# Kernel optimization log

Hardware: AMD Instinct MI355X
Metric: run time of the kernel (lower is better)

The kernel has to match this reference:

```python
import jax, jax.numpy as jnp
import numpy as np


def setup_inputs() -> dict:
    key = jax.random.key(0)
    k1, k2 = jax.random.split(key)
    B, P, D = 32, 1024, 384
    x = jax.random.normal(k1, (B, P, D), dtype=jnp.float32)
    durations = jax.random.randint(k2, (B, P), 0, 8, dtype=jnp.int32)
    return {"x": x, "durations": durations, "max_length": 3072}


def reference(x, durations, max_length):
    # x: [B, P, D], durations: [B, P] int
    B, P, D = x.shape
    csum = jnp.cumsum(durations, axis=1)                       # [B, P] inclusive cumsum
    total = csum[:, -1]
    output_lengths = jnp.minimum(total, max_length).astype(jnp.int32)  # clamp like torch.clamp
    T = max_length  # static: durations are chosen so max(output_lengths) == max_length
    t = jnp.arange(T, dtype=jnp.int32)                         # [T] mel frame positions
    # phoneme index for frame t: smallest j with csum[j] > t (skips zero-duration phonemes)
    idx = jax.vmap(lambda c: jnp.searchsorted(c, t, side='right'))(csum)  # [B, T]
    idx = jnp.clip(idx, 0, P - 1)
    out = jnp.take_along_axis(x, idx[:, :, None], axis=1)      # [B, T, D] gather
    mask = t[None, :] < output_lengths[:, None]                # frames past length stay zero
    out = jnp.where(mask[:, :, None], out, jnp.zeros((), dtype=x.dtype))
    return out, output_lengths
```

## Files before the change

kernel.cpp:

```cpp
#include <hip/hip_runtime.h>


#define BB 32
#define PP 1024
#define DD 384
#define TT 3072

__global__ __launch_bounds__(256) void lr_scan_idx_kernel(
    const int* __restrict__ dur, int* __restrict__ idx_map,
    float* __restrict__ len_out)
{
    __shared__ int csum[PP];
    __shared__ int wtot[4];
    const int b    = blockIdx.x;
    const int tid  = threadIdx.x;
    const int lane = tid & 63;
    const int wave = tid >> 6;

    int4 d = ((const int4*)(dur + b * PP))[tid];
    int s0 = d.x;
    int s1 = s0 + d.y;
    int s2 = s1 + d.z;
    int s3 = s2 + d.w;

    int wsum = s3;
    #pragma unroll
    for (int off = 1; off < 64; off <<= 1) {
        int v = __shfl_up(wsum, off, 64);
        if (lane >= off) wsum += v;
    }
    if (lane == 63) wtot[wave] = wsum;
    __syncthreads();

    int woff = 0;
    for (int w = 0; w < wave; ++w) woff += wtot[w];
    const int pre = woff + wsum - s3;

    csum[tid * 4 + 0] = pre + s0;
    csum[tid * 4 + 1] = pre + s1;
    csum[tid * 4 + 2] = pre + s2;
    csum[tid * 4 + 3] = pre + s3;
    __syncthreads();

    const int total  = csum[PP - 1];
    const int outlen = total < TT ? total : TT;
    if (tid == 0) len_out[b] = (float)outlen;

    for (int t = tid; t < TT; t += 256) {
        int m = -1;
        if (t < outlen) {
            int lo = 0, hi = PP;
            while (lo < hi) {
                int mid = (lo + hi) >> 1;
                if (csum[mid] <= t) lo = mid + 1; else hi = mid;
            }
            m = lo;
        }
        idx_map[b * TT + t] = m;
    }
}

__global__ __launch_bounds__(384) void lr_gather_kernel(
    const float* __restrict__ x, const int* __restrict__ idx_map,
    float* __restrict__ out)
{
    const int j   = threadIdx.x;
    const int lr  = j / 96;
    const int c   = j - lr * 96;
    const int b   = blockIdx.y;
    const int t   = blockIdx.x * 4 + lr;
    const int row = b * TT + t;

    const int m = idx_map[row];
    float4 v = make_float4(0.f, 0.f, 0.f, 0.f);
    if (m >= 0) {
        v = ((const float4*)(x + ((size_t)b * PP + m) * DD))[c];
    }
    ((float4*)out)[(size_t)row * 96 + c] = v;
}

extern "C" void kernel_launch(void* const* d_in, const int* in_sizes, int n_in,
                              void* d_out, int out_size, void* d_ws, size_t ws_size,
                              hipStream_t stream) {
    const float* x   = (const float*)d_in[0];
    const int*   dur = (const int*)d_in[1];

    float* out     = (float*)d_out;
    float* len_out = out + (size_t)BB * TT * DD;
    int*   idx_map = (int*)d_ws;

    lr_scan_idx_kernel<<<BB, 256, 0, stream>>>(dur, idx_map, len_out);
    lr_gather_kernel<<<dim3(TT / 4, BB), 384, 0, stream>>>(x, idx_map, out);
}
```

Before: 204.7 us.

## Fuse duration scan and gather into one chunked kernel with scatter-built index

```diff
diff --git a/kernel.cpp b/kernel.cpp
--- a/kernel.cpp
+++ b/kernel.cpp
@@ -5,78 +5,70 @@
 #define PP 1024
 #define DD 384
 #define TT 3072
+#define NCHUNK 16
+#define CHUNK (TT / NCHUNK)
+#define BLOCK 512
+#define NWAVE (BLOCK / 64)
+#define ROW4 (DD / 4)
 
-__global__ __launch_bounds__(256) void lr_scan_idx_kernel(
-    const int* __restrict__ dur, int* __restrict__ idx_map,
-    float* __restrict__ len_out)
+__global__ __launch_bounds__(BLOCK) void lr_fused_kernel(
+    const float* __restrict__ x, const int* __restrict__ dur,
+    float* __restrict__ out, float* __restrict__ len_out)
 {
-    __shared__ int csum[PP];
-    __shared__ int wtot[4];
-    const int b    = blockIdx.x;
+    __shared__ int lidx[CHUNK];
+    __shared__ int wtot[NWAVE];
+
     const int tid  = threadIdx.x;
     const int lane = tid & 63;
-    const int wave = tid >> 6;
+    const int wv   = tid >> 6;
+    const int b    = blockIdx.y;
+    const int lo   = blockIdx.x * CHUNK;
 
-    int4 d = ((const int4*)(dur + b * PP))[tid];
-    int s0 = d.x;
-    int s1 = s0 + d.y;
-    int s2 = s1 + d.z;
-    int s3 = s2 + d.w;
-
-    int wsum = s3;
+    int2 d = ((const int2*)(dur + b * PP))[tid];
+    const int s = d.x + d.y;
+    int wsum = s;
     #pragma unroll
     for (int off = 1; off < 64; off <<= 1) {
         int v = __shfl_up(wsum, off, 64);
         if (lane >= off) wsum += v;
     }
-    if (lane == 63) wtot[wave] = wsum;
+    if (lane == 63) wtot[wv] = wsum;
+    for (int i = tid; i < CHUNK; i += BLOCK) lidx[i] = -1;
     __syncthreads();
 
-    int woff = 0;
-    for (int w = 0; w < wave; ++w) woff += wtot[w];
-    const int pre = woff + wsum - s3;
+    int woff = 0, total = 0;
+    #pragma unroll
+    for (int w = 0; w < NWAVE; ++w) {
+        int v = wtot[w];
+        if (w < wv) woff += v;
+        total += v;
+    }
+    const int pre    = woff + wsum - s;
+    const int outlen = total < TT ? total : TT;
 
-    csum[tid * 4 + 0] = pre + s0;
-    csum[tid * 4 + 1] = pre + s1;
-    csum[tid * 4 + 2] = pre + s2;
-    csum[tid * 4 + 3] = pre + s3;
+    if (blockIdx.x == 0 && tid == 0) len_out[b] = (float)outlen;
+
+    {
+        const int hi = lo + CHUNK;
+        int a0 = pre, a1 = pre + d.x, a2 = pre + s;
+        int t0 = a0 > lo ? a0 : lo, e0 = a1 < hi ? a1 : hi;
+        for (int t = t0; t < e0; ++t) lidx[t - lo] = 2 * tid;
+        int t1 = a1 > lo ? a1 : lo, e1 = a2 < hi ? a2 : hi;
+        for (int t = t1; t < e1; ++t) lidx[t - lo] = 2 * tid + 1;
+    }
     __syncthreads();
 
-    const int total  = csum[PP - 1];
-    const int outlen = total < TT ? total : TT;
-    if (tid == 0) len_out[b] = (float)outlen;
-
-    for (int t = tid; t < TT; t += 256) {
-        int m = -1;
-        if (t < outlen) {
-            int lo = 0, hi = PP;
-            while (lo < hi) {
-                int mid = (lo + hi) >> 1;
-                if (csum[mid] <= t) lo = mid + 1; else hi = mid;
-            }
-            m = lo;
-        }
-        idx_map[b * TT + t] = m;
+    const float4* __restrict__ x4 = (const float4*)(x + (size_t)b * PP * DD);
+    float4* __restrict__ o4 = (float4*)(out + ((size_t)b * TT + lo) * DD);
+    #pragma unroll 4
+    for (int e = tid; e < CHUNK * ROW4; e += BLOCK) {
+        const int t1 = e / ROW4;
+        const int c  = e - t1 * ROW4;
+        int m = lidx[t1];
+        float4 v = x4[(m < 0 ? 0 : m) * ROW4 + c];
+        if (lo + t1 >= outlen) v = make_float4(0.f, 0.f, 0.f, 0.f);
+        o4[e] = v;
     }
-}
-
-__global__ __launch_bounds__(384) void lr_gather_kernel(
-    const float* __restrict__ x, const int* __restrict__ idx_map,
-    float* __restrict__ out)
-{
-    const int j   = threadIdx.x;
-    const int lr  = j / 96;
-    const int c   = j - lr * 96;
-    const int b   = blockIdx.y;
-    const int t   = blockIdx.x * 4 + lr;
-    const int row = b * TT + t;
-
-    const int m = idx_map[row];
-    float4 v = make_float4(0.f, 0.f, 0.f, 0.f);
-    if (m >= 0) {
-        v = ((const float4*)(x + ((size_t)b * PP + m) * DD))[c];
-    }
-    ((float4*)out)[(size_t)row * 96 + c] = v;
 }
 
 extern "C" void kernel_launch(void* const* d_in, const int* in_sizes, int n_in,
@@ -87,8 +79,6 @@
 
     float* out     = (float*)d_out;
     float* len_out = out + (size_t)BB * TT * DD;
-    int*   idx_map = (int*)d_ws;
 
-    lr_scan_idx_kernel<<<BB, 256, 0, stream>>>(dur, idx_map, len_out);
-    lr_gather_kernel<<<dim3(TT / 4, BB), 384, 0, stream>>>(x, idx_map, out);
+    lr_fused_kernel<<<dim3(NCHUNK, BB), BLOCK, 0, stream>>>(x, dur, out, len_out);
 }
```

Measured after the change: 191.3 us (median of 2 runs). 6.5% less time.
